# Performance work log

Hardware: AMD Instinct MI355X
Metric: run time of the kernel (lower is better)

The kernel has to match this reference:

```python
import jax, jax.numpy as jnp
import numpy as np

B, S, D, H, F = 2, 2048, 1024, 16, 4096
DH = D // H


def setup_inputs() -> dict:
    key = jax.random.key(0)
    ks = jax.random.split(key, 8)
    scale = 0.02
    def nrm(k, shape):
        return jax.random.normal(k, shape, jnp.float32) * scale
    return {
        "x": jax.random.normal(ks[0], (B, S, D), jnp.float32),
        "ln1_g": jnp.ones((D,), jnp.float32),
        "ln1_b": jnp.zeros((D,), jnp.float32),
        "wq": nrm(ks[1], (D, D)), "bq": jnp.zeros((D,), jnp.float32),
        "wk": nrm(ks[2], (D, D)), "bk": jnp.zeros((D,), jnp.float32),
        "wv": nrm(ks[3], (D, D)), "bv": jnp.zeros((D,), jnp.float32),
        "wo": nrm(ks[4], (D, D)), "bo": jnp.zeros((D,), jnp.float32),
        "ln2_g": jnp.ones((D,), jnp.float32),
        "ln2_b": jnp.zeros((D,), jnp.float32),
        "w1": nrm(ks[5], (D, F)), "b1": jnp.zeros((F,), jnp.float32),
        "w2": nrm(ks[6], (F, D)), "b2": jnp.zeros((D,), jnp.float32),
    }


def _layernorm(x, g, b, eps=1e-5):
    m = jnp.mean(x, axis=-1, keepdims=True)
    v = jnp.var(x, axis=-1, keepdims=True)
    return (x - m) / jnp.sqrt(v + eps) * g + b


def reference(x, ln1_g, ln1_b, wq, bq, wk, bk, wv, bv, wo, bo,
              ln2_g, ln2_b, w1, b1, w2, b2):
    # GPT2Block forward, prefill path (state=None): K/V = ln_1(x), causal mask.
    Bx, Sx, Dx = x.shape
    h = _layernorm(x, ln1_g, ln1_b)

    def heads(t):  # [B,S,D] -> [B,H,S,DH]
        return t.reshape(Bx, Sx, H, DH).transpose(0, 2, 1, 3)

    q = heads(h @ wq + bq)
    k = heads(h @ wk + bk)
    v = heads(h @ wv + bv)

    scores = jnp.einsum('bhqd,bhkd->bhqk', q, k) / jnp.sqrt(jnp.float32(DH))
    # masked_softmax: key position < valid_len (= query_pos+1) kept; else -1e6
    causal = jnp.arange(Sx)[None, :] <= jnp.arange(Sx)[:, None]  # [S,S]
    scores = jnp.where(causal, scores, jnp.float32(-1e6))
    attn_w = jax.nn.softmax(scores, axis=-1)

    o = jnp.einsum('bhqk,bhkd->bhqd', attn_w, v)
    o = o.transpose(0, 2, 1, 3).reshape(Bx, Sx, Dx)
    attn_out = o @ wo + bo

    add1 = x + attn_out  # dropout inactive (eval)
    h2 = _layernorm(add1, ln2_g, ln2_b)
    mlp = jax.nn.gelu(h2 @ w1 + b1, approximate=False) @ w2 + b2
    return add1 + mlp
```

## Files before the change

kernel.cpp:

```cpp
#include <hip/hip_runtime.h>
#include <hip/hip_bf16.h>


#define BDIM 1024
#define SEQ 2048
#define NH 16
#define DHEAD 64
#define FDIM 4096
#define QKVD 3072

typedef __attribute__((ext_vector_type(8))) short short8v;
typedef __attribute__((ext_vector_type(4))) float floatx4;

__device__ __forceinline__ unsigned short f2bf(float f) {
    unsigned int u = __float_as_uint(f);
    unsigned int r = u + 0x7FFFu + ((u >> 16) & 1u);
    return (unsigned short)(r >> 16);
}
__device__ __forceinline__ unsigned int pack2bf(float a, float b) {
    return (unsigned int)f2bf(a) | ((unsigned int)f2bf(b) << 16);
}

__device__ __forceinline__ void load16_lds(const unsigned short* g, short* l) {
    __builtin_amdgcn_global_load_lds((const __attribute__((address_space(1))) void*)g,
                                     (__attribute__((address_space(3))) void*)l, 16, 0, 0);
}

__global__ __launch_bounds__(256) void transpose_all(const float* __restrict__ wq,
                                                     const float* __restrict__ wk,
                                                     const float* __restrict__ wv,
                                                     const float* __restrict__ wo,
                                                     const float* __restrict__ w1,
                                                     const float* __restrict__ w2,
                                                     unsigned short* __restrict__ qkvT,
                                                     unsigned short* __restrict__ woT,
                                                     unsigned short* __restrict__ w1T,
                                                     unsigned short* __restrict__ w2T) {
    const int g = blockIdx.x;
    const float* W;
    unsigned short* Wt;
    int K, N, tx, ty;
    if (g < 4096) {
        const int w = g >> 10, tile = g & 1023;
        tx = tile & 31; ty = tile >> 5; K = 1024; N = 1024;
        W = (w == 0) ? wq : (w == 1) ? wk : (w == 2) ? wv : wo;
        Wt = (w == 3) ? woT : qkvT + (size_t)w * 1024 * 1024;
    } else if (g < 8192) {
        const int tile = g - 4096;
        tx = tile & 127; ty = tile >> 7; K = 1024; N = 4096;
        W = w1; Wt = w1T;
    } else {
        const int tile = g - 8192;
        tx = tile & 31; ty = tile >> 5; K = 4096; N = 1024;
        W = w2; Wt = w2T;
    }
    __shared__ float tile[32][33];
    const int t = threadIdx.x;
    const int r = t >> 3, c4 = (t & 7) * 4;
    const int n0 = tx * 32, k0 = ty * 32;
    float4 p = *(const float4*)(W + (size_t)(k0 + r) * N + n0 + c4);
    tile[r][c4 + 0] = p.x;
    tile[r][c4 + 1] = p.y;
    tile[r][c4 + 2] = p.z;
    tile[r][c4 + 3] = p.w;
    __syncthreads();
    ushort4 ou;
    ou.x = f2bf(tile[c4 + 0][r]);
    ou.y = f2bf(tile[c4 + 1][r]);
    ou.z = f2bf(tile[c4 + 2][r]);
    ou.w = f2bf(tile[c4 + 3][r]);
    *(ushort4*)(Wt + (size_t)(n0 + r) * K + k0 + c4) = ou;
}

__global__ void concat_bias(const float* __restrict__ a, const float* __restrict__ b,
                            const float* __restrict__ c, float* __restrict__ out) {
    int i = blockIdx.x * 256 + threadIdx.x;
    out[i] = (i < 1024) ? a[i] : (i < 2048 ? b[i - 1024] : c[i - 2048]);
}

__global__ __launch_bounds__(256) void ln_kernel(const float* __restrict__ x,
                                                 const float* __restrict__ g,
                                                 const float* __restrict__ bb,
                                                 unsigned short* __restrict__ out) {
    const int row = blockIdx.x;
    const int t = threadIdx.x;
    const int c = t * 4;
    float4 p = *(const float4*)(x + (size_t)row * BDIM + c);
    float s = p.x + p.y + p.z + p.w;
    float sq = p.x * p.x + p.y * p.y + p.z * p.z + p.w * p.w;
    for (int off = 1; off < 64; off <<= 1) {
        s += __shfl_xor(s, off);
        sq += __shfl_xor(sq, off);
    }
    __shared__ float ssum[4], ssq[4];
    const int wave = t >> 6, lane = t & 63;
    if (lane == 0) { ssum[wave] = s; ssq[wave] = sq; }
    __syncthreads();
    s = ssum[0] + ssum[1] + ssum[2] + ssum[3];
    sq = ssq[0] + ssq[1] + ssq[2] + ssq[3];
    const float mean = s * (1.0f / BDIM);
    const float var = sq * (1.0f / BDIM) - mean * mean;
    const float rstd = rsqrtf(var + 1e-5f);
    float4 gg = *(const float4*)(g + c);
    float4 bv = *(const float4*)(bb + c);
    ushort4 o;
    o.x = f2bf((p.x - mean) * rstd * gg.x + bv.x);
    o.y = f2bf((p.y - mean) * rstd * gg.y + bv.y);
    o.z = f2bf((p.z - mean) * rstd * gg.z + bv.z);
    o.w = f2bf((p.w - mean) * rstd * gg.w + bv.w);
    *(ushort4*)(out + (size_t)row * BDIM + c) = o;
}

template <int BM, int BN, int BK, int RES, int GELU, int OBF16, int QSCALE = 0, int VOUT = 0, int SWAP = 1>
__global__ __launch_bounds__(256, (BN == 256) ? 2 : 3) void mfma_gemm(
        const unsigned short* __restrict__ A,
        const unsigned short* __restrict__ Bt,
        const float* __restrict__ bias,
        const float* __restrict__ res,
        void* __restrict__ Cv,
        unsigned short* __restrict__ vtout,
        int M, int N, int K) {
    constexpr int HH = BK / 32;
    constexpr int NI = (BN == 256) ? 8 : 4;
    constexpr int MI = (BN >= 128) ? 4 : (BM == 128 ? 2 : 1);
    constexpr int CHA = BM * 4;
    constexpr int CHB = BN * 4;
    __shared__ short As[HH][BM * 32];
    __shared__ short Bs[HH][BN * 32];
    const int t = threadIdx.x;
    const int wave = t >> 6, lane = t & 63;

    const int nwg = gridDim.x * gridDim.y;
    int bid = blockIdx.y * gridDim.x + blockIdx.x;
    bid = (bid & 7) * (nwg >> 3) + (bid >> 3);
    const int bx = bid % gridDim.x, by = bid / gridDim.x;
    const int m0 = by * BM, n0 = bx * BN;

    const int wmrow = (BN >= 128) ? (wave & 1) * 64 : (BM == 128 ? wave * 32 : wave * 16);
    const int wnrow = (BN == 256) ? (wave >> 1) * 128 : ((BN == 128) ? (wave >> 1) * 64 : 0);
    const int mlane = lane & 15, quad = lane >> 4;

    floatx4 acc[MI][NI];
#pragma unroll
    for (int mi = 0; mi < MI; ++mi)
#pragma unroll
        for (int ni = 0; ni < NI; ++ni) {
            floatx4 z = {0.0f, 0.0f, 0.0f, 0.0f};
            acc[mi][ni] = z;
        }

    for (int k0 = 0; k0 < K; k0 += BK) {
        __syncthreads();
#pragma unroll
        for (int j = 0; j < HH * CHA / 256; ++j) {
            const int c = j * 256 + t;
            const int hh = c / CHA, cc = c % CHA;
            load16_lds(A + (size_t)(m0 + (cc >> 2)) * K + k0 + hh * 32 + (cc & 3) * 8,
                       &As[hh][cc * 8]);
        }
#pragma unroll
        for (int j = 0; j < HH * CHB / 256; ++j) {
            const int c = j * 256 + t;
            const int hh = c / CHB, cc = c % CHB;
            load16_lds(Bt + (size_t)(n0 + (cc >> 2)) * K + k0 + hh * 32 + (cc & 3) * 8,
                       &Bs[hh][cc * 8]);
        }
        __syncthreads();
#pragma unroll
        for (int hh = 0; hh < HH; ++hh) {
            short8v a[MI], b[NI];
#pragma unroll
            for (int mi = 0; mi < MI; ++mi)
                a[mi] = *(const short8v*)&As[hh][(wmrow + mi * 16 + mlane) * 32 + quad * 8];
#pragma unroll
            for (int ni = 0; ni < NI; ++ni)
                b[ni] = *(const short8v*)&Bs[hh][(wnrow + ni * 16 + mlane) * 32 + quad * 8];
#pragma unroll
            for (int mi = 0; mi < MI; ++mi)
#pragma unroll
                for (int ni = 0; ni < NI; ++ni) {
                    if (SWAP)
                        acc[mi][ni] = __builtin_amdgcn_mfma_f32_16x16x32_bf16(b[ni], a[mi], acc[mi][ni], 0, 0, 0);
                    else
                        acc[mi][ni] = __builtin_amdgcn_mfma_f32_16x16x32_bf16(a[mi], b[ni], acc[mi][ni], 0, 0, 0);
                }
        }
    }

    if (SWAP) {
#pragma unroll
        for (int mi = 0; mi < MI; ++mi) {
            const int row = m0 + wmrow + mi * 16 + mlane;
#pragma unroll
            for (int ni = 0; ni < NI; ++ni) {
                const int col0 = n0 + wnrow + ni * 16 + quad * 4;
                const float4 bv4 = *(const float4*)(bias + col0);
                float v0 = acc[mi][ni][0] + bv4.x;
                float v1 = acc[mi][ni][1] + bv4.y;
                float v2 = acc[mi][ni][2] + bv4.z;
                float v3 = acc[mi][ni][3] + bv4.w;
                if (RES) {
                    const float4 r4 = *(const float4*)(res + (size_t)row * N + col0);
                    v0 += r4.x; v1 += r4.y; v2 += r4.z; v3 += r4.w;
                }
                if (GELU) {
                    v0 = 0.5f * v0 * (1.0f + erff(v0 * 0.70710678118654752f));
                    v1 = 0.5f * v1 * (1.0f + erff(v1 * 0.70710678118654752f));
                    v2 = 0.5f * v2 * (1.0f + erff(v2 * 0.70710678118654752f));
                    v3 = 0.5f * v3 * (1.0f + erff(v3 * 0.70710678118654752f));
                }
                if (OBF16) {
                    uint2 pk;
                    pk.x = pack2bf(v0, v1);
                    pk.y = pack2bf(v2, v3);
                    *(uint2*)((unsigned short*)Cv + (size_t)row * N + col0) = pk;
                } else {
                    float4 o4 = {v0, v1, v2, v3};
                    *(float4*)((float*)Cv + (size_t)row * N + col0) = o4;
                }
            }
        }
    } else {
#pragma unroll
        for (int mi = 0; mi < MI; ++mi) {
#pragma unroll
            for (int ni = 0; ni < NI; ++ni) {
                const int col = n0 + wnrow + ni * 16 + mlane;
                const float bv = bias[col];
                const int row0 = m0 + wmrow + mi * 16 + quad * 4;
                if (VOUT && col >= 2048) {
                    const int vd = col - 2048;
                    const int bb = row0 >> 11, ss = row0 & 2047;
                    uint2 pk;
                    pk.x = pack2bf(acc[mi][ni][0] + bv, acc[mi][ni][1] + bv);
                    pk.y = pack2bf(acc[mi][ni][2] + bv, acc[mi][ni][3] + bv);
                    *(uint2*)(vtout + ((size_t)(bb * NH + (vd >> 6)) * DHEAD + (vd & 63)) * SEQ + ss) = pk;
                } else {
#pragma unroll
                    for (int rg = 0; rg < 4; ++rg) {
                        const int row = row0 + rg;
                        float v = acc[mi][ni][rg] + bv;
                        if (RES) v += res[(size_t)row * N + col];
                        if (GELU) v = 0.5f * v * (1.0f + erff(v * 0.70710678118654752f));
                        if (QSCALE && col < 1024) v *= 0.18033688011112042f;
                        if (OBF16)
                            ((unsigned short*)Cv)[(size_t)row * N + col] = f2bf(v);
                        else
                            ((float*)Cv)[(size_t)row * N + col] = v;
                    }
                }
            }
        }
    }
}

__global__ __launch_bounds__(512, 4) void attn_kernel(const unsigned short* __restrict__ qkv,
                                                      const unsigned short* __restrict__ vt,
                                                      unsigned short* __restrict__ o) {
    const int g = blockIdx.x;
    const int qt = (g < 256) ? (15 - (g >> 5)) : ((g - 256) >> 5);
    const int hb = g & 31;
    const int h = hb & 15, b = hb >> 4;
    const int t = threadIdx.x;
    const int wave = t >> 6, lane = t & 63;
    const int mlane = lane & 15, quad = lane >> 4;
    const int msw = mlane & 7;
    const int wq0 = qt * 128 + wave * 16;
    const size_t bS = (size_t)b * SEQ;

    __shared__ unsigned short Ks[64][64];
    __shared__ unsigned short Vs[64][64];
    __shared__ __align__(16) unsigned short plds[8][16][64];

    short8v qf0, qf1;
    {
        const unsigned short* qrow = qkv + (bS + wq0 + mlane) * QKVD + h * DHEAD;
        qf0 = *(const short8v*)(qrow + quad * 8);
        qf1 = *(const short8v*)(qrow + 32 + quad * 8);
    }

    const unsigned short* kbase = qkv + bS * QKVD + 1024 + h * DHEAD;
    const unsigned short* vbase = vt + ((size_t)(b * NH + h)) * DHEAD * SEQ;

    const int sr = t >> 3, sc = t & 7;
    const int ssw = (sc ^ (sr & 7)) * 8;
    const unsigned short* kg = kbase + (size_t)sr * QKVD + sc * 8;
    const unsigned short* vg = vbase + (size_t)sr * SEQ + sc * 8;

    floatx4 ot[4];
#pragma unroll
    for (int mt = 0; mt < 4; ++mt) { floatx4 z = {0, 0, 0, 0}; ot[mt] = z; }
    float m_r = -INFINITY, l_r = 0.0f;

    const int kend = wq0 + 16;
    const int kmax = qt * 128 + 128;

    uint4 kr = *(const uint4*)kg;
    uint4 vr = *(const uint4*)vg;

    for (int k0 = 0; k0 < kmax; k0 += 64) {
        *(uint4*)&Ks[sr][ssw] = kr;
        *(uint4*)&Vs[sr][ssw] = vr;
        __syncthreads();
        if (k0 + 64 < kmax) {
            kr = *(const uint4*)(kg + (size_t)(k0 + 64) * QKVD);
            vr = *(const uint4*)(vg + (k0 + 64));
        }
        if (k0 < kend) {
            floatx4 st[4];
#pragma unroll
            for (int kt = 0; kt < 4; ++kt) {
                if (k0 + kt * 16 < kend) {
                    short8v kfa = *(const short8v*)&Ks[kt * 16 + mlane][(quad ^ msw) * 8];
                    short8v kfb = *(const short8v*)&Ks[kt * 16 + mlane][((quad + 4) ^ msw) * 8];
                    floatx4 z = {0, 0, 0, 0};
                    st[kt] = __builtin_amdgcn_mfma_f32_16x16x32_bf16(kfa, qf0, z, 0, 0, 0);
                    st[kt] = __builtin_amdgcn_mfma_f32_16x16x32_bf16(kfb, qf1, st[kt], 0, 0, 0);
                } else {
                    floatx4 mz = {-1e30f, -1e30f, -1e30f, -1e30f};
                    st[kt] = mz;
                }
            }
            if (k0 + 64 >= kend) {
#pragma unroll
                for (int kt = 0; kt < 4; ++kt)
#pragma unroll
                    for (int rg = 0; rg < 4; ++rg)
                        if (k0 + kt * 16 + quad * 4 + rg > wq0 + mlane)
                            st[kt][rg] = -1e30f;
            }
            float tm = st[0][0];
#pragma unroll
            for (int kt = 0; kt < 4; ++kt)
#pragma unroll
                for (int rg = 0; rg < 4; ++rg) tm = fmaxf(tm, st[kt][rg]);
            tm = fmaxf(tm, __shfl_xor(tm, 16));
            tm = fmaxf(tm, __shfl_xor(tm, 32));
            if (!__all(tm <= m_r + 8.0f)) {
                const float newm = fmaxf(m_r, tm);
                const float alpha = exp2f(m_r - newm);
                l_r *= alpha;
#pragma unroll
                for (int mt = 0; mt < 4; ++mt)
#pragma unroll
                    for (int rg = 0; rg < 4; ++rg) ot[mt][rg] *= alpha;
                m_r = newm;
            }
            float p[4][4], psum = 0.0f;
#pragma unroll
            for (int kt = 0; kt < 4; ++kt)
#pragma unroll
                for (int rg = 0; rg < 4; ++rg) {
                    p[kt][rg] = exp2f(st[kt][rg] - m_r);
                    psum += p[kt][rg];
                }
            psum += __shfl_xor(psum, 16);
            psum += __shfl_xor(psum, 32);
            l_r += psum;
            char* prow = (char*)&plds[wave][mlane][0];
#pragma unroll
            for (int kt = 0; kt < 4; ++kt) {
                uint2 pk;
                pk.x = pack2bf(p[kt][0], p[kt][1]);
                pk.y = pack2bf(p[kt][2], p[kt][3]);
                *(uint2*)(prow + ((kt * 32 + quad * 8) ^ (msw << 4))) = pk;
            }
#pragma unroll
            for (int kh = 0; kh < 2; ++kh) {
                if (k0 + kh * 32 < kend) {
                    short8v vf[4];
#pragma unroll
                    for (int mt = 0; mt < 4; ++mt)
                        vf[mt] = *(const short8v*)&Vs[mt * 16 + mlane][(((kh * 4 + quad) ^ msw)) * 8];
                    short8v pf = *(const short8v*)(prow + (((kh * 4 + quad) ^ msw) << 4));
#pragma unroll
                    for (int mt = 0; mt < 4; ++mt)
                        ot[mt] = __builtin_amdgcn_mfma_f32_16x16x32_bf16(vf[mt], pf, ot[mt], 0, 0, 0);
                }
            }
        }
        __syncthreads();
    }

    const float inv = 1.0f / l_r;
    unsigned short* orow = o + (bS + wq0 + mlane) * BDIM + h * DHEAD;
#pragma unroll
    for (int mt = 0; mt < 4; ++mt) {
        uint2 pk;
        pk.x = pack2bf(ot[mt][0] * inv, ot[mt][1] * inv);
        pk.y = pack2bf(ot[mt][2] * inv, ot[mt][3] * inv);
        *(uint2*)(orow + mt * 16 + quad * 4) = pk;
    }
}

extern "C" void kernel_launch(void* const* d_in, const int* in_sizes, int n_in,
                              void* d_out, int out_size, void* d_ws, size_t ws_size,
                              hipStream_t stream) {
    const int M = 2 * SEQ;

    const float* x = (const float*)d_in[0];
    const float* ln1_g = (const float*)d_in[1];
    const float* ln1_b = (const float*)d_in[2];
    const float* wq = (const float*)d_in[3];
    const float* bq = (const float*)d_in[4];
    const float* wk = (const float*)d_in[5];
    const float* bk = (const float*)d_in[6];
    const float* wv = (const float*)d_in[7];
    const float* bv = (const float*)d_in[8];
    const float* wo = (const float*)d_in[9];
    const float* bo = (const float*)d_in[10];
    const float* ln2_g = (const float*)d_in[11];
    const float* ln2_b = (const float*)d_in[12];
    const float* w1 = (const float*)d_in[13];
    const float* b1 = (const float*)d_in[14];
    const float* w2 = (const float*)d_in[15];
    const float* b2 = (const float*)d_in[16];

    char* wsb = (char*)d_ws;
    unsigned short* qkv = (unsigned short*)wsb;
    unsigned short* ffn = (unsigned short*)wsb;
    unsigned short* vt = (unsigned short*)(wsb + (24u << 20));
    unsigned short* hbuf = (unsigned short*)(wsb + (32u << 20));
    float* add1 = (float*)(wsb + (40u << 20));
    unsigned short* h2 = (unsigned short*)(wsb + (56u << 20));
    unsigned short* qkvT = (unsigned short*)(wsb + (64u << 20));
    unsigned short* woT = (unsigned short*)(wsb + (70u << 20));
    unsigned short* w1T = (unsigned short*)(wsb + (72u << 20));
    unsigned short* w2T = (unsigned short*)(wsb + (80u << 20));
    float* bqkv = (float*)(wsb + (88u << 20));

    transpose_all<<<12288, 256, 0, stream>>>(wq, wk, wv, wo, w1, w2, qkvT, woT, w1T, w2T);
    concat_bias<<<12, 256, 0, stream>>>(bq, bk, bv, bqkv);

    ln_kernel<<<M, 256, 0, stream>>>(x, ln1_g, ln1_b, hbuf);

    mfma_gemm<128, 256, 64, 0, 0, 1, 1, 1, 0><<<dim3(QKVD / 256, M / 128), 256, 0, stream>>>(
        hbuf, qkvT, bqkv, nullptr, qkv, vt, M, QKVD, 1024);

    attn_kernel<<<512, 512, 0, stream>>>(qkv, vt, hbuf);

    mfma_gemm<128, 64, 128, 1, 0, 0, 0, 0, 1><<<dim3(1024 / 64, M / 128), 256, 0, stream>>>(
        hbuf, woT, bo, x, add1, nullptr, M, 1024, 1024);

    ln_kernel<<<M, 256, 0, stream>>>(add1, ln2_g, ln2_b, h2);

    mfma_gemm<128, 256, 64, 0, 1, 1, 0, 0, 1><<<dim3(FDIM / 256, M / 128), 256, 0, stream>>>(
        h2, w1T, b1, nullptr, ffn, nullptr, M, FDIM, 1024);

    mfma_gemm<128, 64, 128, 1, 0, 0, 0, 0, 1><<<dim3(1024 / 64, M / 128), 256, 0, stream>>>(
        ffn, w2T, b2, add1, (float*)d_out, nullptr, M, 1024, FDIM);
}
```

Before: 359.4 us.

## Shrink attention blocks to 64 query rows and use hardware bf16 pack

The attention kernel now uses 256-thread blocks covering 64 query rows instead of 512 threads covering 128, doubling the grid to 1024 blocks. Each thread loads two K/V rows per tile so the 64-key tile is still filled. This gives finer causal load balancing and less wasted tail work per block, but K/V tiles are reloaded from global memory by twice as many blocks. Software bf16 rounding is also replaced with the v_cvt_pk_bf16_f32 instruction to cut ALU work in the softmax and output packing.

```diff
diff --git a/kernel.cpp b/kernel.cpp
--- a/kernel.cpp
+++ b/kernel.cpp
@@ -19,6 +19,11 @@
 }
 __device__ __forceinline__ unsigned int pack2bf(float a, float b) {
     return (unsigned int)f2bf(a) | ((unsigned int)f2bf(b) << 16);
+}
+__device__ __forceinline__ unsigned int cvtpk2(float a, float b) {
+    unsigned int r;
+    asm("v_cvt_pk_bf16_f32 %0, %1, %2" : "=v"(r) : "v"(a), "v"(b));
+    return r;
 }
 
 __device__ __forceinline__ void load16_lds(const unsigned short* g, short* l) {
@@ -254,23 +259,23 @@
     }
 }
 
-__global__ __launch_bounds__(512, 4) void attn_kernel(const unsigned short* __restrict__ qkv,
+__global__ __launch_bounds__(256, 4) void attn_kernel(const unsigned short* __restrict__ qkv,
                                                       const unsigned short* __restrict__ vt,
                                                       unsigned short* __restrict__ o) {
     const int g = blockIdx.x;
-    const int qt = (g < 256) ? (15 - (g >> 5)) : ((g - 256) >> 5);
+    const int qt = (g < 512) ? (31 - (g >> 5)) : ((g - 512) >> 5);
     const int hb = g & 31;
     const int h = hb & 15, b = hb >> 4;
     const int t = threadIdx.x;
     const int wave = t >> 6, lane = t & 63;
     const int mlane = lane & 15, quad = lane >> 4;
     const int msw = mlane & 7;
-    const int wq0 = qt * 128 + wave * 16;
+    const int wq0 = qt * 64 + wave * 16;
     const size_t bS = (size_t)b * SEQ;
 
     __shared__ unsigned short Ks[64][64];
     __shared__ unsigned short Vs[64][64];
-    __shared__ __align__(16) unsigned short plds[8][16][64];
+    __shared__ __align__(16) unsigned short plds[4][16][64];
 
     short8v qf0, qf1;
     {
@@ -284,8 +289,10 @@
 
     const int sr = t >> 3, sc = t & 7;
     const int ssw = (sc ^ (sr & 7)) * 8;
-    const unsigned short* kg = kbase + (size_t)sr * QKVD + sc * 8;
-    const unsigned short* vg = vbase + (size_t)sr * SEQ + sc * 8;
+    const unsigned short* kg0 = kbase + (size_t)sr * QKVD + sc * 8;
+    const unsigned short* kg1 = kbase + (size_t)(32 + sr) * QKVD + sc * 8;
+    const unsigned short* vg0 = vbase + (size_t)sr * SEQ + sc * 8;
+    const unsigned short* vg1 = vbase + (size_t)(32 + sr) * SEQ + sc * 8;
 
     floatx4 ot[4];
 #pragma unroll
@@ -293,18 +300,24 @@
     float m_r = -INFINITY, l_r = 0.0f;
 
     const int kend = wq0 + 16;
-    const int kmax = qt * 128 + 128;
-
-    uint4 kr = *(const uint4*)kg;
-    uint4 vr = *(const uint4*)vg;
+    const int kmax = qt * 64 + 64;
+
+    uint4 kr0 = *(const uint4*)kg0;
+    uint4 kr1 = *(const uint4*)kg1;
+    uint4 vr0 = *(const uint4*)vg0;
+    uint4 vr1 = *(const uint4*)vg1;
 
     for (int k0 = 0; k0 < kmax; k0 += 64) {
-        *(uint4*)&Ks[sr][ssw] = kr;
-        *(uint4*)&Vs[sr][ssw] = vr;
+        *(uint4*)&Ks[sr][ssw] = kr0;
+        *(uint4*)&Ks[32 + sr][ssw] = kr1;
+        *(uint4*)&Vs[sr][ssw] = vr0;
+        *(uint4*)&Vs[32 + sr][ssw] = vr1;
         __syncthreads();
         if (k0 + 64 < kmax) {
-            kr = *(const uint4*)(kg + (size_t)(k0 + 64) * QKVD);
-            vr = *(const uint4*)(vg + (k0 + 64));
+            kr0 = *(const uint4*)(kg0 + (size_t)(k0 + 64) * QKVD);
+            kr1 = *(const uint4*)(kg1 + (size_t)(k0 + 64) * QKVD);
+            vr0 = *(const uint4*)(vg0 + (k0 + 64));
+            vr1 = *(const uint4*)(vg1 + (k0 + 64));
         }
         if (k0 < kend) {
             floatx4 st[4];
@@ -361,8 +374,8 @@
 #pragma unroll
             for (int kt = 0; kt < 4; ++kt) {
                 uint2 pk;
-                pk.x = pack2bf(p[kt][0], p[kt][1]);
-                pk.y = pack2bf(p[kt][2], p[kt][3]);
+                pk.x = cvtpk2(p[kt][0], p[kt][1]);
+                pk.y = cvtpk2(p[kt][2], p[kt][3]);
                 *(uint2*)(prow + ((kt * 32 + quad * 8) ^ (msw << 4))) = pk;
             }
 #pragma unroll
@@ -387,8 +400,8 @@
 #pragma unroll
     for (int mt = 0; mt < 4; ++mt) {
         uint2 pk;
-        pk.x = pack2bf(ot[mt][0] * inv, ot[mt][1] * inv);
-        pk.y = pack2bf(ot[mt][2] * inv, ot[mt][3] * inv);
+        pk.x = cvtpk2(ot[mt][0] * inv, ot[mt][1] * inv);
+        pk.y = cvtpk2(ot[mt][2] * inv, ot[mt][3] * inv);
         *(uint2*)(orow + mt * 16 + quad * 4) = pk;
     }
 }
@@ -437,7 +450,7 @@
     mfma_gemm<128, 256, 64, 0, 0, 1, 1, 1, 0><<<dim3(QKVD / 256, M / 128), 256, 0, stream>>>(
         hbuf, qkvT, bqkv, nullptr, qkv, vt, M, QKVD, 1024);
 
-    attn_kernel<<<512, 512, 0, stream>>>(qkv, vt, hbuf);
+    attn_kernel<<<1024, 256, 0, stream>>>(qkv, vt, hbuf);
 
     mfma_gemm<128, 64, 128, 1, 0, 0, 0, 0, 1><<<dim3(1024 / 64, M / 128), 256, 0, stream>>>(
         hbuf, woT, bo, x, add1, nullptr, M, 1024, 1024);
```

New measurement: 350.1 us. 2.6% less time.
